# Performance work log

Hardware: AMD Instinct MI355X
Metric: run time of the kernel (lower is better)

Reference implementation:

```python
import jax, jax.numpy as jnp
import numpy as np


def setup_inputs() -> dict:
    key = jax.random.key(0)
    ks = jax.random.split(key, 6)
    B, H, Tq, Tk, D, HID = 2, 4, 512, 512, 64, 128
    return {
        "q": jax.random.normal(ks[0], (B, H, Tq, D), dtype=jnp.float32),
        "k": jax.random.normal(ks[1], (B, H, Tk, D), dtype=jnp.float32),
        # W1 stored math-layout [Dq+Dk, hidden] (torch Linear weight is its transpose)
        "W1": jax.random.normal(ks[2], (2 * D, HID), dtype=jnp.float32) * (1.0 / np.sqrt(2 * D)),
        "b1": jax.random.normal(ks[3], (HID,), dtype=jnp.float32) * 0.02,
        "W2": jax.random.normal(ks[4], (HID, 1), dtype=jnp.float32) * (1.0 / np.sqrt(HID)),
        "b2": jax.random.normal(ks[5], (1,), dtype=jnp.float32) * 0.02,
    }


def reference(q, k, W1, b1, W2, b2):
    """Pairwise MLP scores s[b,h,i,j] = W2 . relu(W1 @ [q_i; k_j] + b1) + b2.

    Linear over cat(q,k) decomposes into separate q/k projections that are
    broadcast-summed, avoiding the [B,H,Tq,Tk,Dq+Dk] concat tensor (same math).
    """
    Dq = q.shape[-1]
    qh = jnp.einsum("bhqd,dc->bhqc", q, W1[:Dq])   # [B,H,Tq,hid]
    kh = jnp.einsum("bhkd,dc->bhkc", k, W1[Dq:])   # [B,H,Tk,hid]
    h = jax.nn.relu(qh[:, :, :, None, :] + kh[:, :, None, :, :] + b1)  # [B,H,Tq,Tk,hid]
    s = jnp.einsum("bhqkc,c->bhqk", h, W2[:, 0]) + b2[0]
    return s
```

## Files before the change

kernel.cpp:

```cpp
#include <hip/hip_runtime.h>

#define T    512
#define D    64
#define HID  128
#define NBH  8

__global__ __launch_bounds__(256) void proj_kernel(
    const float* __restrict__ q, const float* __restrict__ k,
    const float* __restrict__ W1, const float* __restrict__ b1,
    float* __restrict__ qh_t, float* __restrict__ kh_t)
{
    const int bid   = blockIdx.x;
    const int bh    = bid >> 4;
    const int src   = (bid >> 3) & 1;
    const int chunk = bid & 7;

    const float* __restrict__ X   = (src == 0) ? q : k;
    float* __restrict__ outp      = (src == 0) ? qh_t : kh_t;

    __shared__ float w1t[HID][68];

    const int tid = threadIdx.x;
    for (int idx = tid; idx < D * HID; idx += 256) {
        const int d = idx >> 7;
        const int c = idx & (HID - 1);
        w1t[c][d] = W1[(src * D + d) * HID + c];
    }
    __syncthreads();

    const int r  = tid & 63;
    const int cg = tid >> 6;
    const int i  = chunk * 64 + r;

    float xr[D];
    const float4* xrow = (const float4*)(X + (size_t)(bh * T + i) * D);
    #pragma unroll
    for (int t = 0; t < D / 4; ++t) {
        const float4 v = xrow[t];
        xr[4*t+0] = v.x; xr[4*t+1] = v.y; xr[4*t+2] = v.z; xr[4*t+3] = v.w;
    }

    for (int cc = 0; cc < 32; ++cc) {
        const int c = cg * 32 + cc;
        float acc = (src == 0) ? b1[c] : 0.0f;
        const float4* wrow = (const float4*)(&w1t[c][0]);
        #pragma unroll
        for (int t = 0; t < D / 4; ++t) {
            const float4 w = wrow[t];
            acc += xr[4*t+0]*w.x + xr[4*t+1]*w.y + xr[4*t+2]*w.z + xr[4*t+3]*w.w;
        }
        outp[(size_t)(bh * HID + c) * T + i] = acc;
    }
}

__global__ __launch_bounds__(256) void score_kernel(
    const float* __restrict__ qh_t, const float* __restrict__ kh_t,
    const float* __restrict__ W2, const float* __restrict__ b2,
    float* __restrict__ out)
{
    const int bid = blockIdx.x;
    const int bh  = bid >> 6;
    const int it  = (bid >> 3) & 7;
    const int jt  = bid & 7;
    const int i0  = it * 64;
    const int j0  = jt * 64;

    __shared__ float qt[HID][64];
    __shared__ float kt[HID][64];

    const int tid = threadIdx.x;
    for (int idx = tid; idx < HID * 16; idx += 256) {
        const int c = idx >> 4;
        const int g = idx & 15;
        ((float4*)&qt[c][0])[g] =
            ((const float4*)(qh_t + (size_t)(bh * HID + c) * T + i0))[g];
        ((float4*)&kt[c][0])[g] =
            ((const float4*)(kh_t + (size_t)(bh * HID + c) * T + j0))[g];
    }
    __syncthreads();

    const int tx = tid & 15;
    const int ty = tid >> 4;

    float acc[4][4];
    #pragma unroll
    for (int m = 0; m < 4; ++m)
        #pragma unroll
        for (int n = 0; n < 4; ++n)
            acc[m][n] = 0.0f;

    #pragma unroll 4
    for (int c = 0; c < HID; ++c) {
        const float w = W2[c];
        const float4 qa = ((const float4*)&qt[c][0])[ty];
        const float4 kb = ((const float4*)&kt[c][0])[tx];
        const float qv[4] = {qa.x, qa.y, qa.z, qa.w};
        const float kv[4] = {kb.x, kb.y, kb.z, kb.w};
        #pragma unroll
        for (int m = 0; m < 4; ++m) {
            #pragma unroll
            for (int n = 0; n < 4; ++n) {
                const float u = qv[m] + kv[n];
                acc[m][n] += w * fmaxf(u, 0.0f);
            }
        }
    }

    const float bb = b2[0];
    #pragma unroll
    for (int m = 0; m < 4; ++m) {
        const int i = i0 + 4 * ty + m;
        float4 o;
        o.x = acc[m][0] + bb;
        o.y = acc[m][1] + bb;
        o.z = acc[m][2] + bb;
        o.w = acc[m][3] + bb;
        ((float4*)(out + (size_t)(bh * T + i) * T + j0))[tx] = o;
    }
}

extern "C" void kernel_launch(void* const* d_in, const int* in_sizes, int n_in,
                              void* d_out, int out_size, void* d_ws, size_t ws_size,
                              hipStream_t stream) {
    const float* q  = (const float*)d_in[0];
    const float* k  = (const float*)d_in[1];
    const float* W1 = (const float*)d_in[2];
    const float* b1 = (const float*)d_in[3];
    const float* W2 = (const float*)d_in[4];
    const float* b2 = (const float*)d_in[5];
    float* out = (float*)d_out;

    float* qh_t = (float*)d_ws;
    float* kh_t = qh_t + (size_t)NBH * HID * T;

    proj_kernel<<<128, 256, 0, stream>>>(q, k, W1, b1, qh_t, kh_t);
    score_kernel<<<512, 256, 0, stream>>>(qh_t, kh_t, W2, b2, out);
}
```

Before: 109.0 us.

## Store projections as packed fp16 pairs and score with packed add/max/fdot2

The projection kernel now writes q/k hidden projections as packed half2 pairs of adjacent hidden channels, and is split across twice as many blocks, each covering half the channels. The score kernel loads half-sized tiles and does the pairwise add and relu with packed fp16 ops, then accumulates into fp32 with the fdot2 builtin against fp16-cast W2 pairs. This halves the inner-loop instruction count and the LDS and workspace traffic. The cost is lower precision in the hidden activations and W2 weights, which may push results past the tolerance.

```diff
diff --git a/kernel.cpp b/kernel.cpp
--- a/kernel.cpp
+++ b/kernel.cpp
@@ -4,27 +4,38 @@
 #define D    64
 #define HID  128
 #define NBH  8
+#define NP   (HID / 2)
+
+typedef _Float16 h2 __attribute__((ext_vector_type(2)));
+
+#if __has_builtin(__builtin_amdgcn_fdot2)
+#define HAVE_FDOT2 1
+#else
+#define HAVE_FDOT2 0
+#endif
 
 __global__ __launch_bounds__(256) void proj_kernel(
     const float* __restrict__ q, const float* __restrict__ k,
     const float* __restrict__ W1, const float* __restrict__ b1,
-    float* __restrict__ qh_t, float* __restrict__ kh_t)
+    h2* __restrict__ qh_h, h2* __restrict__ kh_h)
 {
-    const int bid   = blockIdx.x;
-    const int bh    = bid >> 4;
-    const int src   = (bid >> 3) & 1;
-    const int chunk = bid & 7;
+    const int bid    = blockIdx.x;
+    const int bh     = bid >> 5;
+    const int src    = (bid >> 4) & 1;
+    const int chunk  = (bid >> 1) & 7;
+    const int csplit = bid & 1;
+    const int base_c = csplit * 64;
 
-    const float* __restrict__ X   = (src == 0) ? q : k;
-    float* __restrict__ outp      = (src == 0) ? qh_t : kh_t;
+    const float* __restrict__ X = (src == 0) ? q : k;
+    h2* __restrict__ outp       = (src == 0) ? qh_h : kh_h;
 
-    __shared__ float w1t[HID][68];
+    __shared__ float w1t[64][68];
 
     const int tid = threadIdx.x;
-    for (int idx = tid; idx < D * HID; idx += 256) {
-        const int d = idx >> 7;
-        const int c = idx & (HID - 1);
-        w1t[c][d] = W1[(src * D + d) * HID + c];
+    for (int idx = tid; idx < 64 * 64; idx += 256) {
+        const int cc = idx & 63;
+        const int d  = idx >> 6;
+        w1t[cc][d] = W1[(src * D + d) * HID + base_c + cc];
     }
     __syncthreads();
 
@@ -40,21 +51,30 @@
         xr[4*t+0] = v.x; xr[4*t+1] = v.y; xr[4*t+2] = v.z; xr[4*t+3] = v.w;
     }
 
-    for (int cc = 0; cc < 32; ++cc) {
-        const int c = cg * 32 + cc;
-        float acc = (src == 0) ? b1[c] : 0.0f;
-        const float4* wrow = (const float4*)(&w1t[c][0]);
+    #pragma unroll
+    for (int pp = 0; pp < 8; ++pp) {
+        const int cc0 = cg * 16 + 2 * pp;
+        float acc0 = (src == 0) ? b1[base_c + cc0]     : 0.0f;
+        float acc1 = (src == 0) ? b1[base_c + cc0 + 1] : 0.0f;
+        const float4* w0 = (const float4*)(&w1t[cc0][0]);
+        const float4* w1 = (const float4*)(&w1t[cc0 + 1][0]);
         #pragma unroll
         for (int t = 0; t < D / 4; ++t) {
-            const float4 w = wrow[t];
-            acc += xr[4*t+0]*w.x + xr[4*t+1]*w.y + xr[4*t+2]*w.z + xr[4*t+3]*w.w;
+            const float4 a = w0[t];
+            const float4 b = w1[t];
+            acc0 += xr[4*t+0]*a.x + xr[4*t+1]*a.y + xr[4*t+2]*a.z + xr[4*t+3]*a.w;
+            acc1 += xr[4*t+0]*b.x + xr[4*t+1]*b.y + xr[4*t+2]*b.z + xr[4*t+3]*b.w;
         }
-        outp[(size_t)(bh * HID + c) * T + i] = acc;
+        h2 v;
+        v.x = (_Float16)acc0;
+        v.y = (_Float16)acc1;
+        const int p = csplit * 32 + cg * 8 + pp;
+        outp[(size_t)(bh * NP + p) * T + i] = v;
     }
 }
 
 __global__ __launch_bounds__(256) void score_kernel(
-    const float* __restrict__ qh_t, const float* __restrict__ kh_t,
+    const h2* __restrict__ qh_h, const h2* __restrict__ kh_h,
     const float* __restrict__ W2, const float* __restrict__ b2,
     float* __restrict__ out)
 {
@@ -65,17 +85,26 @@
     const int i0  = it * 64;
     const int j0  = jt * 64;
 
-    __shared__ float qt[HID][64];
-    __shared__ float kt[HID][64];
+    __shared__ h2 qt2[NP][64];
+    __shared__ h2 kt2[NP][64];
+    __shared__ h2 w2h[NP];
 
     const int tid = threadIdx.x;
-    for (int idx = tid; idx < HID * 16; idx += 256) {
-        const int c = idx >> 4;
-        const int g = idx & 15;
-        ((float4*)&qt[c][0])[g] =
-            ((const float4*)(qh_t + (size_t)(bh * HID + c) * T + i0))[g];
-        ((float4*)&kt[c][0])[g] =
-            ((const float4*)(kh_t + (size_t)(bh * HID + c) * T + j0))[g];
+    for (int idx = tid; idx < 2 * NP * 16; idx += 256) {
+        const int tile = idx >> 10;
+        const int p    = (idx >> 4) & 63;
+        const int g    = idx & 15;
+        const h2* srcp = tile ? kh_h : qh_h;
+        const int o0   = tile ? j0 : i0;
+        float4 v = ((const float4*)(srcp + (size_t)(bh * NP + p) * T + o0))[g];
+        if (tile) ((float4*)&kt2[p][0])[g] = v;
+        else      ((float4*)&qt2[p][0])[g] = v;
+    }
+    if (tid < NP) {
+        h2 w;
+        w.x = (_Float16)W2[2 * tid];
+        w.y = (_Float16)W2[2 * tid + 1];
+        w2h[tid] = w;
     }
     __syncthreads();
 
@@ -89,19 +118,36 @@
         for (int n = 0; n < 4; ++n)
             acc[m][n] = 0.0f;
 
+    const h2 hzero = (h2)(_Float16)0.0f;
+
     #pragma unroll 4
-    for (int c = 0; c < HID; ++c) {
-        const float w = W2[c];
-        const float4 qa = ((const float4*)&qt[c][0])[ty];
-        const float4 kb = ((const float4*)&kt[c][0])[tx];
-        const float qv[4] = {qa.x, qa.y, qa.z, qa.w};
-        const float kv[4] = {kb.x, kb.y, kb.z, kb.w};
+    for (int p = 0; p < NP; ++p) {
+        const float4 qa4 = ((const float4*)&qt2[p][0])[ty];
+        const float4 kb4 = ((const float4*)&kt2[p][0])[tx];
+        const h2 w = w2h[p];
+        h2 qa[4], kb[4];
+        qa[0] = __builtin_bit_cast(h2, qa4.x);
+        qa[1] = __builtin_bit_cast(h2, qa4.y);
+        qa[2] = __builtin_bit_cast(h2, qa4.z);
+        qa[3] = __builtin_bit_cast(h2, qa4.w);
+        kb[0] = __builtin_bit_cast(h2, kb4.x);
+        kb[1] = __builtin_bit_cast(h2, kb4.y);
+        kb[2] = __builtin_bit_cast(h2, kb4.z);
+        kb[3] = __builtin_bit_cast(h2, kb4.w);
+#if !HAVE_FDOT2
+        const float wx = (float)w.x, wy = (float)w.y;
+#endif
         #pragma unroll
         for (int m = 0; m < 4; ++m) {
             #pragma unroll
             for (int n = 0; n < 4; ++n) {
-                const float u = qv[m] + kv[n];
-                acc[m][n] += w * fmaxf(u, 0.0f);
+                h2 u = qa[m] + kb[n];
+                u = __builtin_elementwise_max(u, hzero);
+#if HAVE_FDOT2
+                acc[m][n] = __builtin_amdgcn_fdot2(u, w, acc[m][n], false);
+#else
+                acc[m][n] += (float)u.x * wx + (float)u.y * wy;
+#endif
             }
         }
     }
@@ -130,9 +176,9 @@
     const float* b2 = (const float*)d_in[5];
     float* out = (float*)d_out;
 
-    float* qh_t = (float*)d_ws;
-    float* kh_t = qh_t + (size_t)NBH * HID * T;
+    h2* qh_h = (h2*)d_ws;
+    h2* kh_h = qh_h + (size_t)NBH * NP * T;
 
-    proj_kernel<<<128, 256, 0, stream>>>(q, k, W1, b1, qh_t, kh_t);
-    score_kernel<<<512, 256, 0, stream>>>(qh_t, kh_t, W2, b2, out);
+    proj_kernel<<<256, 256, 0, stream>>>(q, k, W1, b1, qh_h, kh_h);
+    score_kernel<<<512, 256, 0, stream>>>(qh_h, kh_h, W2, b2, out);
 }
```

New measurement: 92.13 us. 1.18x faster.
